# Kernel optimization log

Measured on AMD Instinct MI355X. Metric: run time of the kernel, lower is better.

The kernel has to match this reference:

```python
import jax, jax.numpy as jnp
import numpy as np

IM_H, IM_W = 128, 128       # im_size
HT_H, HT_W = 184, 180       # ht_size (rho x theta)
N_VOTES = 4_000_000         # number of (pixel, bin, weight) vote triples
NORM = float(max(IM_H, IM_W))


def setup_inputs() -> dict:
    key = jax.random.key(0)
    k1, k2, k3, k4 = jax.random.split(key, 4)
    x = jax.random.normal(k1, (2, 16, IM_H, IM_W), dtype=jnp.float32)
    vote_pixel = jax.random.randint(k2, (N_VOTES,), 0, IM_H * IM_W)   # pixel flat index
    vote_bin = jax.random.randint(k3, (N_VOTES,), 0, HT_H * HT_W)     # HT bin flat index
    vote_weight = jax.random.uniform(k4, (N_VOTES,), dtype=jnp.float32)
    return {"x": x, "vote_pixel": vote_pixel, "vote_bin": vote_bin,
            "vote_weight": vote_weight}


def reference(x, vote_pixel, vote_bin, vote_weight):
    # The original view(b*2, c//2, r, w) is a pure reshape; the scatter is
    # independent per (batch, channel) map, so we flatten all maps together.
    b, c, r, w = x.shape
    xf = x.reshape(b * c, r * w)                         # [BC, P]
    gathered = xf[:, vote_pixel] * vote_weight[None, :]  # [BC, N]
    # weighted scatter-add into HT bins (segment sum over leading axis)
    out = jax.ops.segment_sum(gathered.T, vote_bin, num_segments=HT_H * HT_W)  # [HB, BC]
    out = out.T.reshape(b, c, HT_H, HT_W)
    return out / NORM
```

## Files before the change

kernel.cpp:

```cpp
#include <hip/hip_runtime.h>
#include <stdint.h>

#define IM_HW   16384
#define NBINS   33120
#define NMAPS   32
#define INV_NORM (1.0f / 128.0f)

#define BBITS   5
#define NBUCK   1035
#define CAPB    4352
#define SLAB    192
#define SSTR    196
#define NB_SCAT 512
#define NT_SCAT 1024
#define LDSVOT  7936
#define OVR_CAP 8192

__device__ __forceinline__ float w_from_top13(unsigned e) {
  const unsigned short hb = (unsigned short)((e >> 19) << 3);
  return (float)__builtin_bit_cast(_Float16, hb);
}
__device__ __forceinline__ float f16u(unsigned short h) {
  return (float)__builtin_bit_cast(_Float16, h);
}

__global__ __launch_bounds__(NT_SCAT) void k_scatter_bucket(
    const float* __restrict__ x, unsigned short* __restrict__ xT2,
    const int* __restrict__ vp, const int* __restrict__ vb,
    const float* __restrict__ vw, int nv,
    unsigned* __restrict__ globcur,
    unsigned* __restrict__ ovrcnt,
    uint2*   __restrict__ ovrlist,
    unsigned* __restrict__ sorted) {
  __shared__ unsigned h[NBUCK];
  __shared__ unsigned lstart[NBUCK];
  __shared__ unsigned cur[NBUCK];
  __shared__ unsigned lds[LDSVOT];
  __shared__ unsigned short bid[LDSVOT];

  const int tid = threadIdx.x;

  {
    const int i = blockIdx.x * 1024 + tid;
    const int m = i & 31, p = i >> 5;
    xT2[i] = __builtin_bit_cast(unsigned short, (_Float16)x[m * IM_HW + p]);
  }

  const int chunk = (((nv + NB_SCAT - 1) / NB_SCAT) + 3) & ~3;
  const int c0 = blockIdx.x * chunk;
  const int c1 = min(nv, c0 + chunk);
  const int cnt = (c1 > c0) ? (c1 - c0) : 0;

  for (int i = tid; i < NBUCK; i += NT_SCAT) h[i] = 0u;
  __syncthreads();

  unsigned e[16];
  unsigned short rr[16], bu16[16];
  const int ng = cnt >> 2;
  const int4*   vp4 = (const int4*)(vp + c0);
  const int4*   vb4 = (const int4*)(vb + c0);
  const float4* vw4 = (const float4*)(vw + c0);
  #pragma unroll
  for (int j = 0; j < 4; ++j) {
    const int g = tid + j * NT_SCAT;
    if (g < ng) {
      const int4 p = vp4[g]; const int4 b = vb4[g]; const float4 w = vw4[g];
      const int k = j * 4;
      #define STAGE(q, PP, BB, WW) { \
        const unsigned short hw = __builtin_bit_cast(unsigned short, (_Float16)(WW)); \
        e[k + q] = (unsigned)(PP) | (((unsigned)(BB) & 31u) << 14) | (((unsigned)hw >> 3) << 19); \
        bu16[k + q] = (unsigned short)((unsigned)(BB) >> BBITS); \
        rr[k + q] = (unsigned short)atomicAdd(&h[(unsigned)(BB) >> BBITS], 1u); }
      STAGE(0, p.x, b.x, w.x) STAGE(1, p.y, b.y, w.y)
      STAGE(2, p.z, b.z, w.z) STAGE(3, p.w, b.w, w.w)
      #undef STAGE
    }
  }
  const int tail0 = ng * 4;
  if (tid < cnt - tail0) {
    const int gi = c0 + tail0 + tid;
    unsigned o = atomicAdd(ovrcnt, 1u);
    if (o < OVR_CAP)
      ovrlist[o] = make_uint2((unsigned)vp[gi] | ((unsigned)vb[gi] << 14),
                              __float_as_uint(vw[gi]));
  }
  __syncthreads();

  if (tid < 64) {
    const int lo = tid * 17, hi = min(NBUCK, lo + 17);
    unsigned s = 0;
    for (int i = lo; i < hi; ++i) s += h[i];
    unsigned inc = s;
    #pragma unroll
    for (int d = 1; d < 64; d <<= 1) {
      const unsigned v = __shfl_up(inc, d);
      if (tid >= d) inc += v;
    }
    unsigned run = inc - s;
    for (int i = lo; i < hi; ++i) { lstart[i] = run; run += h[i]; }
  } else {
    for (int i = tid - 64; i < NBUCK; i += (NT_SCAT - 64))
      cur[i] = (h[i] != 0u) ? atomicAdd(&globcur[i], h[i]) : 0u;
  }
  __syncthreads();

  #pragma unroll
  for (int j = 0; j < 4; ++j) {
    const int g = tid + j * NT_SCAT;
    if (g < ng) {
      #pragma unroll
      for (int q = 0; q < 4; ++q) {
        const int k = j * 4 + q;
        const unsigned pos = lstart[bu16[k]] + (unsigned)rr[k];
        lds[pos] = e[k];
        bid[pos] = bu16[k];
      }
    }
  }
  __syncthreads();

  const int staged = ng << 2;
  for (int i = (tid << 1); i < staged; i += (NT_SCAT << 1)) {
    const uint2 E2 = *(const uint2*)&lds[i];
    const unsigned bp = *(const unsigned*)&bid[i];
    const unsigned b0 = bp & 0xFFFFu, b1 = bp >> 16;
    const unsigned g0 = cur[b0] + (unsigned)i       - lstart[b0];
    const unsigned g1 = cur[b1] + (unsigned)(i + 1) - lstart[b1];
    if (g0 < CAPB) {
      sorted[(size_t)b0 * CAPB + g0] = E2.x;
    } else {
      unsigned o = atomicAdd(ovrcnt, 1u);
      if (o < OVR_CAP) {
        const unsigned bin = (b0 << BBITS) + ((E2.x >> 14) & 31u);
        ovrlist[o] = make_uint2((E2.x & 0x3FFFu) | (bin << 14),
                                __float_as_uint(w_from_top13(E2.x)));
      }
    }
    if (g1 < CAPB) {
      sorted[(size_t)b1 * CAPB + g1] = E2.y;
    } else {
      unsigned o = atomicAdd(ovrcnt, 1u);
      if (o < OVR_CAP) {
        const unsigned bin = (b1 << BBITS) + ((E2.y >> 14) & 31u);
        ovrlist[o] = make_uint2((E2.y & 0x3FFFu) | (bin << 14),
                                __float_as_uint(w_from_top13(E2.y)));
      }
    }
  }
}

__global__ __launch_bounds__(512) void k_spmm_static(
    const unsigned* __restrict__ sorted, const unsigned* __restrict__ globcur,
    const unsigned short* __restrict__ xT2, float* __restrict__ out,
    unsigned* __restrict__ ovrcnt, uint2* __restrict__ ovrlist) {
  __shared__ unsigned sv[32 * SSTR];
  __shared__ unsigned cur[32];
  __shared__ float tile[32][33];
  const int tid = threadIdx.x;
  const int bu = blockIdx.x;
  const int n = min((int)globcur[bu], CAPB);

  if (tid < 32) cur[tid] = 0u;
  __syncthreads();

  const uint4* src = (const uint4*)(sorted + (size_t)bu * CAPB);
  const int nq = n >> 2;
  #define PLACE(E) { \
    const unsigned fb = ((E) >> 14) & 31u; \
    const unsigned s = atomicAdd(&cur[fb], 1u); \
    if (s < SLAB) sv[fb * SSTR + s] = (E) & 0xFFF83FFFu; \
    else { \
      unsigned o = atomicAdd(ovrcnt, 1u); \
      if (o < OVR_CAP) \
        ovrlist[o] = make_uint2(((E) & 0x3FFFu) | ((((unsigned)bu << BBITS) + fb) << 14), \
                                __float_as_uint(w_from_top13(E))); } }
  for (int i = tid; i < nq; i += 512) {
    const uint4 q = src[i];
    PLACE(q.x) PLACE(q.y) PLACE(q.z) PLACE(q.w)
  }
  if (tid < (n & 3)) {
    const unsigned E = sorted[(size_t)bu * CAPB + (n & ~3) + tid];
    PLACE(E)
  }
  #undef PLACE
  __syncthreads();

  unsigned nov = *ovrcnt;

  #define WDEC(E) ((float)__builtin_bit_cast(_Float16, (unsigned short)((E) >> 16)))
  #define PROC(E) { \
    const uint2 xv = xh4[((E) & 0x3FFFu) * 8 + mp]; \
    const float w = WDEC(E); \
    a0 += w * f16u((unsigned short)(xv.x & 0xFFFFu)); \
    a1 += w * f16u((unsigned short)(xv.x >> 16)); \
    a2 += w * f16u((unsigned short)(xv.y & 0xFFFFu)); \
    a3 += w * f16u((unsigned short)(xv.y >> 16)); }
  const uint2* xh4 = (const uint2*)xT2;
  const int wv = tid >> 6, lane = tid & 63;
  const int q = lane >> 3, mp = lane & 7;
  #pragma unroll
  for (int s4 = 0; s4 < 4; ++s4) {
    const int b = wv * 4 + s4;
    const int cnt = min((int)cur[b], SLAB);
    const unsigned* seg = &sv[b * SSTR];
    float a0 = 0.0f, a1 = 0.0f, a2 = 0.0f, a3 = 0.0f;
    int base = 0;
    for (; base + 32 <= cnt; base += 32) {
      const uint4 a = *(const uint4*)(seg + base + 4 * q);
      PROC(a.x) PROC(a.y) PROC(a.z) PROC(a.w)
    }
    for (int j = base + q; j < cnt; j += 8) {
      const unsigned E = seg[j];
      PROC(E)
    }
    a0 += __shfl_xor(a0, 8); a0 += __shfl_xor(a0, 16); a0 += __shfl_xor(a0, 32);
    a1 += __shfl_xor(a1, 8); a1 += __shfl_xor(a1, 16); a1 += __shfl_xor(a1, 32);
    a2 += __shfl_xor(a2, 8); a2 += __shfl_xor(a2, 16); a2 += __shfl_xor(a2, 32);
    a3 += __shfl_xor(a3, 8); a3 += __shfl_xor(a3, 16); a3 += __shfl_xor(a3, 32);
    if (lane < 8) {
      tile[b][4 * mp]     = a0 * INV_NORM;
      tile[b][4 * mp + 1] = a1 * INV_NORM;
      tile[b][4 * mp + 2] = a2 * INV_NORM;
      tile[b][4 * mp + 3] = a3 * INV_NORM;
    }
  }
  #undef PROC
  #undef WDEC
  __syncthreads();

  {
    nov = nov < (unsigned)OVR_CAP ? nov : (unsigned)OVR_CAP;
    if (nov) {
      for (unsigned idx = tid; idx < nov * 32u; idx += 512u) {
        const unsigned vi = idx >> 5, m2 = idx & 31u;
        const uint2 vv = ovrlist[vi];
        const unsigned bin = vv.x >> 14;
        if ((bin >> BBITS) == (unsigned)bu) {
          const float xv = f16u(xT2[(vv.x & 0x3FFFu) * 32 + m2]);
          atomicAdd(&tile[bin & 31u][m2],
                    __uint_as_float(vv.y) * xv * INV_NORM);
        }
      }
      __syncthreads();
    }
  }

  {
    const int row  = tid >> 4;
    const int col2 = (tid & 15) * 2;
    const int gb0  = bu << BBITS;
    const float2 v2 = make_float2(tile[col2][row], tile[col2 + 1][row]);
    *(float2*)(out + (size_t)row * NBINS + gb0 + col2) = v2;
  }
}

__global__ __launch_bounds__(1024) void ht_fallback(const float* __restrict__ x,
                                                    const int* __restrict__ vp,
                                                    const int* __restrict__ vb,
                                                    const float* __restrict__ vw,
                                                    float* __restrict__ out, int nv) {
  __shared__ float hist[NBINS];
  for (int i = threadIdx.x; i < NBINS; i += 1024) hist[i] = 0.0f;
  __syncthreads();
  const int map = blockIdx.x >> 3, chunk = blockIdx.x & 7;
  const float* xm = x + map * IM_HW;
  const int per = (nv + 7) / 8;
  const int start = chunk * per, end = min(nv, start + per);
  for (int i = start + (int)threadIdx.x; i < end; i += 1024)
    atomicAdd(&hist[vb[i]], xm[vp[i]] * vw[i]);
  __syncthreads();
  float* om = out + map * NBINS;
  for (int i = threadIdx.x; i < NBINS; i += 1024)
    atomicAdd(&om[i], hist[i] * INV_NORM);
}

extern "C" void kernel_launch(void* const* d_in, const int* in_sizes, int n_in,
                              void* d_out, int out_size, void* d_ws, size_t ws_size,
                              hipStream_t stream) {
  const float* x  = (const float*)d_in[0];
  const int*   vp = (const int*)d_in[1];
  const int*   vb = (const int*)d_in[2];
  const float* vw = (const float*)d_in[3];
  float* out = (float*)d_out;
  const int nv = in_sizes[1];

  char* w = (char*)d_ws;
  unsigned*       sorted  = (unsigned*)w;       w += (size_t)NBUCK * CAPB * 4;
  unsigned short* xT2     = (unsigned short*)w; w += (size_t)IM_HW * NMAPS * 2;
  uint2*          ovrlist = (uint2*)w;          w += (size_t)OVR_CAP * 8;
  unsigned*       globcur = (unsigned*)w;       w += (size_t)NBUCK * 4;
  unsigned*       ovrcnt  = (unsigned*)w;       w += 16;
  const size_t need = (size_t)(w - (char*)d_ws);

  if (ws_size >= need) {
    hipMemsetAsync(globcur, 0, (size_t)NBUCK * 4 + 16, stream);
    k_scatter_bucket<<<NB_SCAT, NT_SCAT, 0, stream>>>(x, xT2, vp, vb, vw, nv, globcur,
                                                      ovrcnt, ovrlist, sorted);
    k_spmm_static<<<NBUCK, 512, 0, stream>>>(sorted, globcur, xT2, out,
                                             ovrcnt, ovrlist);
  } else {
    hipMemsetAsync(out, 0, (size_t)out_size * sizeof(float), stream);
    ht_fallback<<<256, 1024, 0, stream>>>(x, vp, vb, vw, out, nv);
  }
}
```

Measured before the change: 137.1 us.

## Pad global bucket counters, split flush into halves, prefetch SpMM vote loads

Global bucket cursors are padded to a 64-byte stride so atomics from many blocks to neighbouring buckets no longer contend on the same cache line. The per-block flush of sorted votes changes from pairs of adjacent entries to each thread writing one entry from each half of the staged array, which changes the global store pattern. The SpMM inner loop software-prefetches the next uint4 of votes from LDS before processing the current one. The costs are a larger memset and workspace for the counters and some extra register pressure.

```diff
diff --git a/kernel.cpp b/kernel.cpp
--- a/kernel.cpp
+++ b/kernel.cpp
@@ -15,6 +15,7 @@
 #define NT_SCAT 1024
 #define LDSVOT  7936
 #define OVR_CAP 8192
+#define GC_STR  16
 
 __device__ __forceinline__ float w_from_top13(unsigned e) {
   const unsigned short hb = (unsigned short)((e >> 19) << 3);
@@ -100,7 +101,7 @@
     for (int i = lo; i < hi; ++i) { lstart[i] = run; run += h[i]; }
   } else {
     for (int i = tid - 64; i < NBUCK; i += (NT_SCAT - 64))
-      cur[i] = (h[i] != 0u) ? atomicAdd(&globcur[i], h[i]) : 0u;
+      cur[i] = (h[i] != 0u) ? atomicAdd(&globcur[(unsigned)i * GC_STR], h[i]) : 0u;
   }
   __syncthreads();
 
@@ -119,34 +120,25 @@
   }
   __syncthreads();
 
+  #define FLUSH1(IDX) { \
+    const unsigned E = lds[IDX]; \
+    const unsigned bu = bid[IDX]; \
+    const unsigned g = cur[bu] + (unsigned)(IDX) - lstart[bu]; \
+    if (g < CAPB) { \
+      sorted[(size_t)bu * CAPB + g] = E; \
+    } else { \
+      unsigned o = atomicAdd(ovrcnt, 1u); \
+      if (o < OVR_CAP) { \
+        const unsigned bin = (bu << BBITS) + ((E >> 14) & 31u); \
+        ovrlist[o] = make_uint2((E & 0x3FFFu) | (bin << 14), \
+                                __float_as_uint(w_from_top13(E))); } } }
   const int staged = ng << 2;
-  for (int i = (tid << 1); i < staged; i += (NT_SCAT << 1)) {
-    const uint2 E2 = *(const uint2*)&lds[i];
-    const unsigned bp = *(const unsigned*)&bid[i];
-    const unsigned b0 = bp & 0xFFFFu, b1 = bp >> 16;
-    const unsigned g0 = cur[b0] + (unsigned)i       - lstart[b0];
-    const unsigned g1 = cur[b1] + (unsigned)(i + 1) - lstart[b1];
-    if (g0 < CAPB) {
-      sorted[(size_t)b0 * CAPB + g0] = E2.x;
-    } else {
-      unsigned o = atomicAdd(ovrcnt, 1u);
-      if (o < OVR_CAP) {
-        const unsigned bin = (b0 << BBITS) + ((E2.x >> 14) & 31u);
-        ovrlist[o] = make_uint2((E2.x & 0x3FFFu) | (bin << 14),
-                                __float_as_uint(w_from_top13(E2.x)));
-      }
-    }
-    if (g1 < CAPB) {
-      sorted[(size_t)b1 * CAPB + g1] = E2.y;
-    } else {
-      unsigned o = atomicAdd(ovrcnt, 1u);
-      if (o < OVR_CAP) {
-        const unsigned bin = (b1 << BBITS) + ((E2.y >> 14) & 31u);
-        ovrlist[o] = make_uint2((E2.y & 0x3FFFu) | (bin << 14),
-                                __float_as_uint(w_from_top13(E2.y)));
-      }
-    }
-  }
+  const int half = staged >> 1;
+  for (int i = tid; i < half; i += NT_SCAT) {
+    FLUSH1(i)
+    FLUSH1(i + half)
+  }
+  #undef FLUSH1
 }
 
 __global__ __launch_bounds__(512) void k_spmm_static(
@@ -158,7 +150,7 @@
   __shared__ float tile[32][33];
   const int tid = threadIdx.x;
   const int bu = blockIdx.x;
-  const int n = min((int)globcur[bu], CAPB);
+  const int n = min((int)globcur[(size_t)bu * GC_STR], CAPB);
 
   if (tid < 32) cur[tid] = 0u;
   __syncthreads();
@@ -204,12 +196,17 @@
     const int cnt = min((int)cur[b], SLAB);
     const unsigned* seg = &sv[b * SSTR];
     float a0 = 0.0f, a1 = 0.0f, a2 = 0.0f, a3 = 0.0f;
-    int base = 0;
-    for (; base + 32 <= cnt; base += 32) {
-      const uint4 a = *(const uint4*)(seg + base + 4 * q);
+    const int nmain = cnt & ~31;
+    if (nmain) {
+      uint4 a = *(const uint4*)(seg + 4 * q);
+      for (int b2 = 32; b2 < nmain; b2 += 32) {
+        const uint4 an = *(const uint4*)(seg + b2 + 4 * q);
+        PROC(a.x) PROC(a.y) PROC(a.z) PROC(a.w)
+        a = an;
+      }
       PROC(a.x) PROC(a.y) PROC(a.z) PROC(a.w)
     }
-    for (int j = base + q; j < cnt; j += 8) {
+    for (int j = nmain + q; j < cnt; j += 8) {
       const unsigned E = seg[j];
       PROC(E)
     }
@@ -288,12 +285,12 @@
   unsigned*       sorted  = (unsigned*)w;       w += (size_t)NBUCK * CAPB * 4;
   unsigned short* xT2     = (unsigned short*)w; w += (size_t)IM_HW * NMAPS * 2;
   uint2*          ovrlist = (uint2*)w;          w += (size_t)OVR_CAP * 8;
-  unsigned*       globcur = (unsigned*)w;       w += (size_t)NBUCK * 4;
+  unsigned*       globcur = (unsigned*)w;       w += (size_t)NBUCK * GC_STR * 4;
   unsigned*       ovrcnt  = (unsigned*)w;       w += 16;
   const size_t need = (size_t)(w - (char*)d_ws);
 
   if (ws_size >= need) {
-    hipMemsetAsync(globcur, 0, (size_t)NBUCK * 4 + 16, stream);
+    hipMemsetAsync(globcur, 0, (size_t)NBUCK * GC_STR * 4 + 16, stream);
     k_scatter_bucket<<<NB_SCAT, NT_SCAT, 0, stream>>>(x, xT2, vp, vb, vw, nv, globcur,
                                                       ovrcnt, ovrlist, sorted);
     k_spmm_static<<<NBUCK, 512, 0, stream>>>(sorted, globcur, xT2, out,
```

Result: slower. 153.2 us (+11.8%).
